# Kernel optimization log

Hardware: AMD Instinct MI355X
Metric: run time of the kernel (lower is better)

Reference implementation:

```python
import jax, jax.numpy as jnp
import numpy as np

E = 8          # num_experts
K = 2          # top_k
R = 16         # lora_r
SCALING = 32.0 / 16.0  # lora_alpha / lora_r

B, S, H, I = 2, 2048, 2048, 8192


def setup_inputs() -> dict:
    key = jax.random.key(0)
    ks = jax.random.split(key, 11)
    inv_h = 1.0 / np.sqrt(H)
    inv_i = 1.0 / np.sqrt(I)
    return {
        "x": jax.random.normal(ks[0], (B, S, H), jnp.float32),
        "gate_W": jax.random.normal(ks[1], (I, H), jnp.float32) * inv_h,
        "up_W": jax.random.normal(ks[2], (I, H), jnp.float32) * inv_h,
        "down_W": jax.random.normal(ks[3], (H, I), jnp.float32) * inv_i,
        "router_W": jax.random.normal(ks[4], (E, H), jnp.float32) * 0.02,
        "gate_A": jax.random.normal(ks[5], (E, R, H), jnp.float32) * inv_h,
        "gate_B": jax.random.normal(ks[6], (E, I, R), jnp.float32) * 0.01,
        "up_A": jax.random.normal(ks[7], (E, R, H), jnp.float32) * inv_h,
        "up_B": jax.random.normal(ks[8], (E, I, R), jnp.float32) * 0.01,
        "down_A": jax.random.normal(ks[9], (E, R, I), jnp.float32) * inv_i,
        "down_B": jax.random.normal(ks[10], (E, H, R), jnp.float32) * 0.01,
    }


def _mixlora_forward(x, gate_W, up_W, down_W, router_W,
                     gate_A, gate_B, up_A, up_B, down_A, down_B):
    b, s, h = x.shape
    T = b * s
    xf = x.reshape(T, h)                                  # [T, H]

    # Shared base FFN projections (computed once for all experts)
    gate_out = xf @ gate_W.T                              # [T, I]
    up_out = xf @ up_W.T                                  # [T, I]

    # Router: softmax in fp32, top-k, renormalize selected weights
    logits = xf @ router_W.T                              # [T, E]
    probs = jax.nn.softmax(logits.astype(jnp.float32), axis=-1)
    w, idx = jax.lax.top_k(probs, K)                      # [T, K]
    w = w / jnp.sum(w, axis=-1, keepdims=True)

    # Dense per-(token, expert) combine weights; 0 for unselected experts
    onehot = jax.nn.one_hot(idx, E, dtype=probs.dtype)    # [T, K, E]
    w_dense = jnp.einsum('tke,tk->te', onehot, w)         # [T, E]

    # Load-balance aux loss: N * sum_i f_i * P_i
    f_i = jnp.sum(onehot, axis=(0, 1)) / T
    p_i = jnp.mean(probs, axis=0)
    aux_loss = E * jnp.dot(f_i, p_i)

    # Scan over experts, accumulating weighted intermediate and down-delta.
    # Since down_proj is linear, sum_k w_k * down(inter_k) = down(sum_k w_k * inter_k).
    def step(carry, p):
        acc_int, acc_dd = carry
        gA, gB, uA, uB, dA, dB, we = p                    # we: [T]
        gd = ((xf @ gA.T) @ gB.T) * SCALING               # [T, I]
        ud = ((xf @ uA.T) @ uB.T) * SCALING               # [T, I]
        inter = jax.nn.silu(gate_out + gd) * (up_out + ud)  # SwiGLU intermediate
        dd = ((inter @ dA.T) @ dB.T) * SCALING            # [T, H]
        we = we.astype(xf.dtype)[:, None]
        return (acc_int + we * inter, acc_dd + we * dd), None

    init = (jnp.zeros((T, gate_W.shape[0]), xf.dtype),
            jnp.zeros((T, h), xf.dtype))
    (acc_int, acc_dd), _ = jax.lax.scan(
        step, init, (gate_A, gate_B, up_A, up_B, down_A, down_B, w_dense.T))

    out = acc_int @ down_W.T + acc_dd                     # [T, H]
    return out.reshape(b, s, h), aux_loss


def reference(x, gate_W, up_W, down_W, router_W,
              gate_A, gate_B, up_A, up_B, down_A, down_B):
    return _mixlora_forward(x, gate_W, up_W, down_W, router_W,
                            gate_A, gate_B, up_A, up_B, down_A, down_B)
```

## Files before the change

### kernel.cpp

```cpp
#include <hip/hip_runtime.h>
#include <stdint.h>
#include <stddef.h>

#define DEVINL __device__ __forceinline__

typedef short sv8 __attribute__((ext_vector_type(8)));
typedef unsigned short usv8 __attribute__((ext_vector_type(8)));
typedef unsigned short usv4 __attribute__((ext_vector_type(4)));
typedef float f32x4 __attribute__((ext_vector_type(4)));

constexpr int T_TOK = 4096;
constexpr int H_DIM = 2048;
constexpr int I_DIM = 8192;
constexpr int E_NUM = 8;
constexpr int R_LORA = 16;
constexpr float SCALING = 2.0f;
constexpr int NQ = 4;
constexpr int TQ = T_TOK / NQ;
constexpr int PQ = TQ * 2;
constexpr int P_TOT = T_TOK * 2;

DEVINL float bf2f(unsigned short u) {
  union { uint32_t i; float f; } v; v.i = ((uint32_t)u) << 16; return v.f;
}
DEVINL unsigned short f2bf(float x) {
  union { float f; uint32_t i; } v; v.f = x;
  uint32_t r = v.i + 0x7FFFu + ((v.i >> 16) & 1u);
  return (unsigned short)(r >> 16);
}
DEVINL float bflo(uint32_t w) {
  union { uint32_t i; float f; } v; v.i = w << 16; return v.f;
}
DEVINL float bfhi(uint32_t w) {
  union { uint32_t i; float f; } v; v.i = w & 0xFFFF0000u; return v.f;
}

DEVINL f32x4 MFMA_BF16(sv8 a, sv8 b, f32x4 c) {
  return __builtin_amdgcn_mfma_f32_16x16x32_bf16(a, b, c, 0, 0, 0);
}

DEVINL void load16_to_lds(const void* g, void* l) {
  __builtin_amdgcn_global_load_lds(
      (const __attribute__((address_space(1))) uint32_t*)g,
      (__attribute__((address_space(3))) uint32_t*)l, 16, 0, 0);
}

#define BARRIER() __builtin_amdgcn_s_barrier()

__global__ void cast_f32_to_bf16(const float4* __restrict__ src, usv4* __restrict__ dst) {
  long i = (long)blockIdx.x * blockDim.x + threadIdx.x;
  float4 v = src[i];
  usv4 o;
  o[0] = f2bf(v.x); o[1] = f2bf(v.y); o[2] = f2bf(v.z); o[3] = f2bf(v.w);
  dst[i] = o;
}

__global__ void cast2_f32_to_bf16(const float4* __restrict__ src0, usv4* __restrict__ dst0,
                                  const float4* __restrict__ src1, usv4* __restrict__ dst1) {
  long i = (long)blockIdx.x * blockDim.x + threadIdx.x;
  const float4* s = blockIdx.y ? src1 : src0;
  usv4* d = blockIdx.y ? dst1 : dst0;
  float4 v = s[i];
  usv4 o;
  o[0] = f2bf(v.x); o[1] = f2bf(v.y); o[2] = f2bf(v.z); o[3] = f2bf(v.w);
  d[i] = o;
}

__global__ void zero_lcnt(int* lcnt) {
  if (threadIdx.x < E_NUM * NQ) lcnt[threadIdx.x] = 0;
}

__global__ void router_kernel(const float* __restrict__ x, const float* __restrict__ rW,
                              float* __restrict__ wbuf, int* __restrict__ idxb,
                              float* __restrict__ probs, int* __restrict__ lcnt,
                              int* __restrict__ lists, unsigned short* __restrict__ xf_bf) {
  const int wave = threadIdx.x >> 6, lane = threadIdx.x & 63;
  const int t = blockIdx.x * 4 + wave;
  const float* xr = x + (long)t * H_DIM;
  unsigned short* xbr = xf_bf + (long)t * H_DIM;
  float acc[E_NUM];
#pragma unroll
  for (int e = 0; e < E_NUM; ++e) acc[e] = 0.f;
  for (int h = lane; h < H_DIM; h += 64) {
    float xv = xr[h];
    xbr[h] = f2bf(xv);
#pragma unroll
    for (int e = 0; e < E_NUM; ++e) acc[e] += xv * rW[e * H_DIM + h];
  }
#pragma unroll
  for (int e = 0; e < E_NUM; ++e) {
#pragma unroll
    for (int off = 32; off; off >>= 1) acc[e] += __shfl_xor(acc[e], off);
  }
  if (lane == 0) {
    float mx = acc[0];
#pragma unroll
    for (int e = 1; e < E_NUM; ++e) mx = fmaxf(mx, acc[e]);
    float p[E_NUM];
    float s = 0.f;
#pragma unroll
    for (int e = 0; e < E_NUM; ++e) { p[e] = expf(acc[e] - mx); s += p[e]; }
    float inv = 1.f / s;
#pragma unroll
    for (int e = 0; e < E_NUM; ++e) p[e] *= inv;
    int e1 = 0;
    for (int e = 1; e < E_NUM; ++e) if (p[e] > p[e1]) e1 = e;
    int e2 = (e1 == 0) ? 1 : 0;
    for (int e = 0; e < E_NUM; ++e) if (e != e1 && p[e] > p[e2]) e2 = e;
    float w1 = p[e1], w2 = p[e2], wsum = w1 + w2;
    wbuf[t * 2 + 0] = w1 / wsum;
    wbuf[t * 2 + 1] = w2 / wsum;
    idxb[t * 2 + 0] = e1;
    idxb[t * 2 + 1] = e2;
#pragma unroll
    for (int e = 0; e < E_NUM; ++e) probs[(long)t * E_NUM + e] = p[e];
    const int q = t / TQ;
    int p1 = atomicAdd(&lcnt[e1 * NQ + q], 1); lists[(e1 * NQ + q) * TQ + p1] = t * 2 + 0;
    int p2 = atomicAdd(&lcnt[e2 * NQ + q], 1); lists[(e2 * NQ + q) * TQ + p2] = t * 2 + 1;
  }
}

__global__ void aux_kernel(const float* __restrict__ probs, const int* __restrict__ lcnt,
                           float* __restrict__ aux_out) {
  const int lane = threadIdx.x;
  float s[E_NUM];
#pragma unroll
  for (int e = 0; e < E_NUM; ++e) s[e] = 0.f;
  for (int t = lane; t < T_TOK; t += 64) {
#pragma unroll
    for (int e = 0; e < E_NUM; ++e) s[e] += probs[(long)t * E_NUM + e];
  }
#pragma unroll
  for (int e = 0; e < E_NUM; ++e) {
#pragma unroll
    for (int off = 32; off; off >>= 1) s[e] += __shfl_xor(s[e], off);
  }
  if (lane == 0) {
    float a = 0.f;
#pragma unroll
    for (int e = 0; e < E_NUM; ++e) {
      int cnt = 0;
#pragma unroll
      for (int q = 0; q < NQ; ++q) cnt += lcnt[e * NQ + q];
      a += ((float)cnt / (float)T_TOK) * (s[e] / (float)T_TOK);
    }
    *aux_out = (float)E_NUM * a;
  }
}

__global__ __launch_bounds__(256)
void lora_a_mfma_kernel(const unsigned short* __restrict__ xf_bf,
                        const unsigned short* __restrict__ gA_bf,
                        const unsigned short* __restrict__ uA_bf,
                        const int* __restrict__ lists, const int* __restrict__ lcnt,
                        float* __restrict__ vg, float* __restrict__ vu) {
  const int q = blockIdx.x / (E_NUM * 16);
  const int rem = blockIdx.x % (E_NUM * 16);
  const int e = rem >> 4;
  const int wave = threadIdx.x >> 6, lane = threadIdx.x & 63;
  const int grp = (rem & 15) * 4 + wave;
  const int npairs = lcnt[e * NQ + q];
  if (grp * 16 >= npairs) return;
  const int* lst = lists + (e * NQ + q) * TQ;
  const int slot = lane & 15;
  int pidx = grp * 16 + slot;
  int pair = lst[(pidx < npairs) ? pidx : grp * 16];
  int t = pair >> 1;
  const long kb = (long)blockIdx.y * 1024 + (lane >> 4) * 8;
  const unsigned short* arow = xf_bf + (long)t * H_DIM + kb;
  const unsigned short* bg = gA_bf + ((long)e * R_LORA + slot) * H_DIM + kb;
  const unsigned short* bu = uA_bf + ((long)e * R_LORA + slot) * H_DIM + kb;
  f32x4 ag = {}, au = {};
#pragma unroll 4
  for (int k = 0; k < 1024; k += 32) {
    sv8 a = *(const sv8*)(arow + k);
    ag = MFMA_BF16(a, *(const sv8*)(bg + k), ag);
    au = MFMA_BF16(a, *(const sv8*)(bu + k), au);
  }
  const int orow = (lane >> 4) * 4;
  const long base = (long)blockIdx.y * P_TOT;
#pragma unroll
  for (int rg = 0; rg < 4; ++rg) {
    int pidx2 = grp * 16 + orow + rg;
    if (pidx2 < npairs) {
      int pr = lst[pidx2];
      vg[(base + pr) * R_LORA + slot] = ag[rg];
      vu[(base + pr) * R_LORA + slot] = au[rg];
    }
  }
}

__global__ void reduce_uguu_kernel(const float* __restrict__ vg, const float* __restrict__ vu,
                                   float* __restrict__ ug, float* __restrict__ uu) {
  long i = (long)blockIdx.x * 256 + threadIdx.x;
  ug[i] = vg[i] + vg[(long)P_TOT * R_LORA + i];
  uu[i] = vu[i] + vu[(long)P_TOT * R_LORA + i];
}

template <bool F32OUT>
__global__ __launch_bounds__(512, 2)
void gemm8p_t(const unsigned short* __restrict__ A,
              const unsigned short* __restrict__ B0,
              const unsigned short* __restrict__ B1,
              unsigned short* __restrict__ Cb0,
              unsigned short* __restrict__ Cb1,
              float* __restrict__ Cf,
              int K, int lda, int ldb, int ldc,
              int az_off, int bz_off, long cz_off) {
  extern __shared__ unsigned short lds[];
  const int z = blockIdx.z;
  const unsigned short* __restrict__ Ap = A + (long)z * az_off;
  const unsigned short* __restrict__ Bp = (z ? B1 : B0) + (long)z * bz_off;
  const int tid = threadIdx.x;
  const int wave = tid >> 6, lane = tid & 63;
  const int wm = wave >> 2, wn = wave & 3;
  const long m0 = (long)blockIdx.y * 256;
  const long n0 = (long)blockIdx.x * 256;
  const int NT = K >> 6;

  const int lr = lane & 15;
  const int lc = (lane >> 4) * 8;
  const int xm = ((lane & 4) << 3) | ((lane & 2) << 3) | ((lane & 1) << 6);
  const int srow = tid >> 3;
  const int scol = (tid & 7) * 8;
  const int gcol = scol ^ (((tid >> 5) & 1) << 4) ^ (((tid >> 4) & 1) << 3)
                        ^ (((tid >> 3) & 1) << 5);

  f32x4 acc[8][4] = {};
  sv8 aF[4][2], bF[4][2];

  auto ldsAt = [&](int buf, int mat) -> unsigned short* {
    return lds + (((buf << 1) + mat) << 14);
  };
  auto stageA = [&](int buf, int R, long k0) {
    load16_to_lds(Ap + (m0 + R + srow) * (long)lda + k0 + gcol,
                  ldsAt(buf, 0) + ((R + srow) << 6) + scol);
  };
  auto stageB = [&](int buf, int R, long k0) {
    load16_to_lds(Bp + (n0 + R + srow) * (long)ldb + k0 + gcol,
                  ldsAt(buf, 1) + ((R + srow) << 6) + scol);
  };
  auto rdA = [&](int buf, int row16, int ks) -> sv8 {
    int bo = ((((row16 + lr) << 7) + ((ks * 32 + lc) << 1))) ^ xm;
    return *(const sv8*)((const char*)ldsAt(buf, 0) + bo);
  };
  auto rdB = [&](int buf, int row16, int ks) -> sv8 {
    int bo = ((((row16 + lr) << 7) + ((ks * 32 + lc) << 1))) ^ xm;
    return *(const sv8*)((const char*)ldsAt(buf, 1) + bo);
  };

  stageA(0, 0, 0); stageA(0, 64, 0); stageA(0, 128, 0); stageA(0, 192, 0);
  stageB(0, 0, 0); stageB(0, 64, 0); stageB(0, 128, 0); stageB(0, 192, 0);
  if (NT > 1) {
    stageA(1, 0, 64); stageA(1, 128, 64);
    asm volatile("s_waitcnt vmcnt(2)" ::: "memory");
  } else {
    asm volatile("s_waitcnt vmcnt(0)" ::: "memory");
  }
  BARRIER();

  for (int t = 0; t < NT; ++t) {
    const int P = t & 1, Q = P ^ 1;
    const long kQ = ((long)t + 1) << 6;
    const long kP2 = ((long)t + 2) << 6;
    const bool hQ = (t + 1) < NT, hP2 = (t + 2) < NT;

#pragma unroll
    for (int mf = 0; mf < 4; ++mf)
#pragma unroll
      for (int ks = 0; ks < 2; ++ks)
        aF[mf][ks] = rdA(P, wm * 128 + mf * 16, ks);
#pragma unroll
    for (int nf = 0; nf < 4; ++nf)
#pragma unroll
      for (int ks = 0; ks < 2; ++ks)
        bF[nf][ks] = rdB(P, wn * 64 + nf * 16, ks);
    if (hQ) { stageA(Q, 64, kQ); stageA(Q, 192, kQ); stageB(Q, 0, kQ); stageB(Q, 64, kQ); }
    __builtin_amdgcn_s_setprio(1);
#pragma unroll
    for (int mf = 0; mf < 4; ++mf)
#pragma unroll
      for (int nf = 0; nf < 4; ++nf)
#pragma unroll
        for (int ks = 0; ks < 2; ++ks)
          acc[mf][nf] = MFMA_BF16(aF[mf][ks], bF[nf][ks], acc[mf][nf]);
    __builtin_amdgcn_s_setprio(0);
    BARRIER();

#pragma unroll
    for (int mf = 0; mf < 4; ++mf)
#pragma unroll
      for (int ks = 0; ks < 2; ++ks)
        aF[mf][ks] = rdA(P, wm * 128 + 64 + mf * 16, ks);
    if (hQ) { stageB(Q, 128, kQ); stageB(Q, 192, kQ); }
    if (hP2) { stageA(P, 0, kP2); stageA(P, 128, kP2); }
    __builtin_amdgcn_s_setprio(1);
#pragma unroll
    for (int mf = 0; mf < 4; ++mf)
#pragma unroll
      for (int nf = 0; nf < 4; ++nf)
#pragma unroll
        for (int ks = 0; ks < 2; ++ks)
          acc[4 + mf][nf] = MFMA_BF16(aF[mf][ks], bF[nf][ks], acc[4 + mf][nf]);
    __builtin_amdgcn_s_setprio(0);
    if (hP2) {
      asm volatile("s_waitcnt vmcnt(2)" ::: "memory");
    } else {
      asm volatile("s_waitcnt vmcnt(0)" ::: "memory");
    }
    BARRIER();
  }

  const int rb = (lane >> 4) * 4, cb = lane & 15;
  if constexpr (F32OUT) {
    float* __restrict__ Cp = Cf + (long)z * cz_off;
#pragma unroll
    for (int mf = 0; mf < 8; ++mf)
#pragma unroll
      for (int nf = 0; nf < 4; ++nf) {
        long col = n0 + wn * 64 + nf * 16 + cb;
#pragma unroll
        for (int r = 0; r < 4; ++r) {
          long row = m0 + wm * 128 + mf * 16 + rb + r;
          Cp[row * ldc + col] = acc[mf][nf][r];
        }
      }
  } else {
    unsigned short* __restrict__ Cp = z ? Cb1 : Cb0;
#pragma unroll
    for (int mf = 0; mf < 8; ++mf)
#pragma unroll
      for (int nf = 0; nf < 4; ++nf) {
        long col = n0 + wn * 64 + nf * 16 + cb;
#pragma unroll
        for (int r = 0; r < 4; ++r) {
          long row = m0 + wm * 128 + mf * 16 + rb + r;
          Cp[row * ldc + col] = f2bf(acc[mf][nf][r]);
        }
      }
  }
}

__global__ __launch_bounds__(256)
void combine2_kernel(const unsigned short* __restrict__ g_bf,
                     const unsigned short* __restrict__ u_bf,
                     const unsigned short* __restrict__ gBp, const unsigned short* __restrict__ uBp,
                     const float* __restrict__ ug, const float* __restrict__ uu,
                     const float* __restrict__ wbuf,
                     const int* __restrict__ lists, const int* __restrict__ lcnt,
                     unsigned short* __restrict__ winter, int q) {
  const int e = blockIdx.y >> 4, chunk = blockIdx.y & 15;
  const int npairs = lcnt[e * NQ + q];
  const int pbase = chunk * 64;
  if (pbase >= npairs) return;
  const int wave = threadIdx.x >> 6, lane = threadIdx.x & 63;
  const long i0 = (long)blockIdx.x * 256 + lane * 4;
  uint32_t gbp[32], ubp[32];
#pragma unroll
  for (int j = 0; j < 4; ++j) {
    const uint4* gp = (const uint4*)(gBp + ((long)e * I_DIM + i0 + j) * R_LORA);
    const uint4* up = (const uint4*)(uBp + ((long)e * I_DIM + i0 + j) * R_LORA);
    uint4 g0 = gp[0], g1 = gp[1], u0 = up[0], u1 = up[1];
    gbp[j * 8 + 0] = g0.x; gbp[j * 8 + 1] = g0.y; gbp[j * 8 + 2] = g0.z; gbp[j * 8 + 3] = g0.w;
    gbp[j * 8 + 4] = g1.x; gbp[j * 8 + 5] = g1.y; gbp[j * 8 + 6] = g1.z; gbp[j * 8 + 7] = g1.w;
    ubp[j * 8 + 0] = u0.x; ubp[j * 8 + 1] = u0.y; ubp[j * 8 + 2] = u0.z; ubp[j * 8 + 3] = u0.w;
    ubp[j * 8 + 4] = u1.x; ubp[j * 8 + 5] = u1.y; ubp[j * 8 + 6] = u1.z; ubp[j * 8 + 7] = u1.w;
  }
  for (int pl = 0; pl < 16; ++pl) {
    int pi = pbase + wave + pl * 4;
    if (pi >= npairs) break;
    int pair = lists[(e * NQ + q) * TQ + pi];
    int t = pair >> 1, plocal = pair - q * PQ;
    float w = wbuf[pair];
    const float2* ug2 = (const float2*)(ug + (long)pair * R_LORA);
    const float2* uu2 = (const float2*)(uu + (long)pair * R_LORA);
    usv4 gv = *(const usv4*)(g_bf + (long)t * I_DIM + i0);
    usv4 uv = *(const usv4*)(u_bf + (long)t * I_DIM + i0);
    float gd[4] = {0.f, 0.f, 0.f, 0.f}, ud[4] = {0.f, 0.f, 0.f, 0.f};
#pragma unroll
    for (int c = 0; c < 8; ++c) {
      float2 a = ug2[c], b = uu2[c];
#pragma unroll
      for (int j = 0; j < 4; ++j) {
        uint32_t gw = gbp[j * 8 + c], uw = ubp[j * 8 + c];
        gd[j] += a.x * bflo(gw) + a.y * bfhi(gw);
        ud[j] += b.x * bflo(uw) + b.y * bfhi(uw);
      }
    }
    usv4 o;
#pragma unroll
    for (int j = 0; j < 4; ++j) {
      float zg = bf2f(gv[j]) + SCALING * gd[j];
      float zu = bf2f(uv[j]) + SCALING * ud[j];
      float sil = zg / (1.f + __expf(-zg));
      o[j] = f2bf(w * sil * zu);
    }
    *(usv4*)(winter + (long)plocal * I_DIM + i0) = o;
  }
}

__global__ void acc_kernel(const unsigned short* __restrict__ winter,
                           unsigned short* __restrict__ acc_bf, int q) {
  long gid = (long)blockIdx.x * 256 + threadIdx.x;
  int tl = (int)(gid >> 10);
  int ig = (int)(gid & 1023);
  int t = q * TQ + tl;
  usv8 a = *(const usv8*)(winter + ((long)(tl * 2 + 0)) * I_DIM + ig * 8);
  usv8 b = *(const usv8*)(winter + ((long)(tl * 2 + 1)) * I_DIM + ig * 8);
  usv8 o;
#pragma unroll
  for (int j = 0; j < 8; ++j) o[j] = f2bf(bf2f(a[j]) + bf2f(b[j]));
  *(usv8*)(acc_bf + (long)t * I_DIM + ig * 8) = o;
}

__global__ __launch_bounds__(256)
void lorav_mfma_kernel(const unsigned short* __restrict__ winter,
                       const unsigned short* __restrict__ dA_bf,
                       const int* __restrict__ lists, const int* __restrict__ lcnt,
                       float* __restrict__ vv, int q) {
  const int e = blockIdx.x >> 4;
  const int wave = threadIdx.x >> 6, lane = threadIdx.x & 63;
  const int grp = (blockIdx.x & 15) * 4 + wave;
  const int npairs = lcnt[e * NQ + q];
  if (grp * 16 >= npairs) return;
  const int* lst = lists + (e * NQ + q) * TQ;
  const int slot = lane & 15;
  int pidx = grp * 16 + slot;
  int pair = lst[(pidx < npairs) ? pidx : grp * 16];
  int plocal = pair - q * PQ;
  const long kb = (long)blockIdx.y * 1024 + (lane >> 4) * 8;
  const unsigned short* arow = winter + (long)plocal * I_DIM + kb;
  const unsigned short* brow = dA_bf + ((long)e * R_LORA + slot) * I_DIM + kb;
  f32x4 acc = {};
#pragma unroll 4
  for (int k = 0; k < 1024; k += 32)
    acc = MFMA_BF16(*(const sv8*)(arow + k), *(const sv8*)(brow + k), acc);
  const int orow = (lane >> 4) * 4;
  const long base = (long)blockIdx.y * P_TOT;
#pragma unroll
  for (int rg = 0; rg < 4; ++rg) {
    int pidx2 = grp * 16 + orow + rg;
    if (pidx2 < npairs) {
      int pr = lst[pidx2];
      vv[(base + pr) * R_LORA + slot] = acc[rg];
    }
  }
}

__global__ void reduce_v_kernel(const float* __restrict__ vv, float* __restrict__ vbuf) {
  long i = (long)blockIdx.x * 256 + threadIdx.x;
  float s = 0.f;
#pragma unroll
  for (int kc = 0; kc < 8; ++kc) s += vv[(long)kc * P_TOT * R_LORA + i];
  vbuf[i] = s;
}

__global__ void ddmerge_kernel(const float* __restrict__ vbuf, const int* __restrict__ idxb,
                               const float* __restrict__ dB,
                               const float* __restrict__ p0, const float* __restrict__ p1,
                               float* __restrict__ out) {
  const int t = blockIdx.y;
  const int h = blockIdx.x * 256 + threadIdx.x;
  const int e0 = idxb[t * 2 + 0], e1 = idxb[t * 2 + 1];
  const float4* v0p = (const float4*)(vbuf + (long)(t * 2 + 0) * R_LORA);
  const float4* v1p = (const float4*)(vbuf + (long)(t * 2 + 1) * R_LORA);
  const float4* b0 = (const float4*)(dB + ((long)e0 * H_DIM + h) * R_LORA);
  const float4* b1 = (const float4*)(dB + ((long)e1 * H_DIM + h) * R_LORA);
  float dd = 0.f;
#pragma unroll
  for (int qq = 0; qq < 4; ++qq) {
    float4 v0 = v0p[qq], x0 = b0[qq];
    float4 v1 = v1p[qq], x1 = b1[qq];
    dd += v0.x * x0.x + v0.y * x0.y + v0.z * x0.z + v0.w * x0.w;
    dd += v1.x * x1.x + v1.y * x1.y + v1.z * x1.z + v1.w * x1.w;
  }
  long i = (long)t * H_DIM + h;
  out[i] = SCALING * dd + p0[i] + p1[i];
}

extern "C" void kernel_launch(void* const* d_in, const int* in_sizes, int n_in,
                              void* d_out, int out_size, void* d_ws, size_t ws_size,
                              hipStream_t stream) {
  (void)in_sizes; (void)n_in; (void)out_size;
  const float* x        = (const float*)d_in[0];
  const float* gate_W   = (const float*)d_in[1];
  const float* up_W     = (const float*)d_in[2];
  const float* down_W   = (const float*)d_in[3];
  const float* router_W = (const float*)d_in[4];
  const float* gate_A   = (const float*)d_in[5];
  const float* gate_B   = (const float*)d_in[6];
  const float* up_A     = (const float*)d_in[7];
  const float* up_B     = (const float*)d_in[8];
  const float* down_A   = (const float*)d_in[9];
  const float* down_B   = (const float*)d_in[10];
  float* out = (float*)d_out;

  char* ws = (char*)d_ws;
  size_t off = 0;
  auto take = [&](size_t bytes) -> char* {
    char* p = ws + off;
    off += (bytes + 255) & ~(size_t)255;
    return p;
  };
  unsigned short* xf_bf  = (unsigned short*)take((size_t)T_TOK * H_DIM * 2);
  unsigned short* gW_bf  = (unsigned short*)take((size_t)I_DIM * H_DIM * 2);
  unsigned short* uW_bf  = (unsigned short*)take((size_t)I_DIM * H_DIM * 2);
  unsigned short* dA_bf  = (unsigned short*)take((size_t)E_NUM * R_LORA * I_DIM * 2);
  unsigned short* g_bf   = (unsigned short*)take((size_t)T_TOK * I_DIM * 2);
  unsigned short* u_bf   = (unsigned short*)take((size_t)T_TOK * I_DIM * 2);
  unsigned short* winterQ= (unsigned short*)take((size_t)PQ * I_DIM * 2);
  float* wbuf  = (float*)take((size_t)P_TOT * 4);
  int*   idxb  = (int*)take((size_t)P_TOT * 4);
  float* ug    = (float*)take((size_t)P_TOT * R_LORA * 4);
  float* uu    = (float*)take((size_t)P_TOT * R_LORA * 4);
  float* vbuf  = (float*)take((size_t)P_TOT * R_LORA * 4);
  float* probs = (float*)take((size_t)T_TOK * E_NUM * 4);
  int*   lcnt  = (int*)take((size_t)E_NUM * NQ * 4);
  int*   lists = (int*)take((size_t)E_NUM * NQ * TQ * 4);

  unsigned short* dW_bf  = gW_bf;
  unsigned short* acc_bf = g_bf;
  float* vg = (float*)winterQ;
  float* vu = (float*)(winterQ + (size_t)1 * 1024 * 1024 / 2);
  unsigned short* gA_bf = winterQ + (size_t)2 * 1024 * 1024 / 2;
  unsigned short* uA_bf = winterQ + (size_t)5 * 512 * 1024 / 2;
  float* vv = (float*)xf_bf;
  unsigned short* gB_bf = (unsigned short*)((char*)xf_bf + ((size_t)4 << 20));
  unsigned short* uB_bf = (unsigned short*)((char*)xf_bf + ((size_t)8 << 20));
  float* pbuf = (float*)u_bf;

  if (ws_size < off) return;

  zero_lcnt<<<1, 64, 0, stream>>>(lcnt);
  router_kernel<<<T_TOK / 4, 256, 0, stream>>>(x, router_W, wbuf, idxb, probs, lcnt, lists, xf_bf);
  aux_kernel<<<1, 64, 0, stream>>>(probs, lcnt, out + (size_t)T_TOK * H_DIM);

  cast2_f32_to_bf16<<<dim3((E_NUM * R_LORA * H_DIM / 4) / 256, 2), 256, 0, stream>>>(
      (const float4*)gate_A, (usv4*)gA_bf, (const float4*)up_A, (usv4*)uA_bf);
  lora_a_mfma_kernel<<<dim3(NQ * E_NUM * 16, 2), 256, 0, stream>>>(xf_bf, gA_bf, uA_bf, lists, lcnt, vg, vu);
  reduce_uguu_kernel<<<(P_TOT * R_LORA) / 256, 256, 0, stream>>>(vg, vu, ug, uu);

  cast2_f32_to_bf16<<<dim3((I_DIM * H_DIM / 4) / 256, 2), 256, 0, stream>>>(
      (const float4*)gate_W, (usv4*)gW_bf, (const float4*)up_W, (usv4*)uW_bf);
  cast_f32_to_bf16<<<(E_NUM * R_LORA * I_DIM / 4) / 256, 256, 0, stream>>>((const float4*)down_A, (usv4*)dA_bf);

  hipFuncSetAttribute(reinterpret_cast<const void*>(&gemm8p_t<false>),
                      hipFuncAttributeMaxDynamicSharedMemorySize, 131072);
  hipFuncSetAttribute(reinterpret_cast<const void*>(&gemm8p_t<true>),
                      hipFuncAttributeMaxDynamicSharedMemorySize, 131072);
  gemm8p_t<false><<<dim3(I_DIM / 256, T_TOK / 256, 2), 512, 131072, stream>>>(
      xf_bf, gW_bf, uW_bf, g_bf, u_bf, nullptr,
      H_DIM, H_DIM, H_DIM, I_DIM, 0, 0, 0);

  cast_f32_to_bf16<<<(H_DIM * I_DIM / 4) / 256, 256, 0, stream>>>((const float4*)down_W, (usv4*)dW_bf);
  cast2_f32_to_bf16<<<dim3((E_NUM * I_DIM * R_LORA / 4) / 256, 2), 256, 0, stream>>>(
      (const float4*)gate_B, (usv4*)gB_bf, (const float4*)up_B, (usv4*)uB_bf);

  for (int q = 0; q < NQ; ++q) {
    combine2_kernel<<<dim3(I_DIM / 256, E_NUM * 16), 256, 0, stream>>>(
        g_bf, u_bf, gB_bf, uB_bf, ug, uu, wbuf, lists, lcnt, winterQ, q);
    acc_kernel<<<(TQ * (I_DIM / 8)) / 256, 256, 0, stream>>>(winterQ, acc_bf, q);
    lorav_mfma_kernel<<<dim3(E_NUM * 16, 8), 256, 0, stream>>>(winterQ, dA_bf, lists, lcnt, vv, q);
  }
  reduce_v_kernel<<<(P_TOT * R_LORA) / 256, 256, 0, stream>>>(vv, vbuf);

  gemm8p_t<true><<<dim3(H_DIM / 256, T_TOK / 256, 2), 512, 131072, stream>>>(
      acc_bf, dW_bf, dW_bf, nullptr, nullptr, pbuf,
      I_DIM / 2, I_DIM, I_DIM, H_DIM, I_DIM / 2, I_DIM / 2, (long)T_TOK * H_DIM);

  ddmerge_kernel<<<dim3(H_DIM / 256, T_TOK), 256, 0, stream>>>(
      vbuf, idxb, down_B, (const float*)pbuf,
      (const float*)(pbuf + (size_t)T_TOK * H_DIM), out);
}
```

Before: 1.043 ms.

## Batch token quarters into single launches and issue all B-tile loads earlier

When the workspace is large enough, the combine, accumulate and LoRA-down kernels now process all four token quarters in one launch each, using blockIdx.z and a winter buffer that is four times larger. This replaces twelve small launches with three larger ones. It cuts launch overhead and the idle gaps between kernels, and it gives each launch more parallel work. The GEMM mainloop also issues all four B-tile stage loads in the first half of each iteration instead of splitting them across the two halves, which changes how prefetch overlaps with the MFMA work.

Measured after the change: 1.039 ms. Within noise of the previous version (-0.3%).

```diff
diff --git a/kernel.cpp b/kernel.cpp
--- a/kernel.cpp
+++ b/kernel.cpp
@@ -275,7 +275,10 @@
 #pragma unroll
       for (int ks = 0; ks < 2; ++ks)
         bF[nf][ks] = rdB(P, wn * 64 + nf * 16, ks);
-    if (hQ) { stageA(Q, 64, kQ); stageA(Q, 192, kQ); stageB(Q, 0, kQ); stageB(Q, 64, kQ); }
+    if (hQ) {
+      stageA(Q, 64, kQ); stageA(Q, 192, kQ);
+      stageB(Q, 0, kQ); stageB(Q, 64, kQ); stageB(Q, 128, kQ); stageB(Q, 192, kQ);
+    }
     __builtin_amdgcn_s_setprio(1);
 #pragma unroll
     for (int mf = 0; mf < 4; ++mf)
@@ -292,7 +295,6 @@
 #pragma unroll
       for (int ks = 0; ks < 2; ++ks)
         aF[mf][ks] = rdA(P, wm * 128 + 64 + mf * 16, ks);
-    if (hQ) { stageB(Q, 128, kQ); stageB(Q, 192, kQ); }
     if (hP2) { stageA(P, 0, kP2); stageA(P, 128, kP2); }
     __builtin_amdgcn_s_setprio(1);
 #pragma unroll
@@ -348,7 +350,10 @@
                      const float* __restrict__ ug, const float* __restrict__ uu,
                      const float* __restrict__ wbuf,
                      const int* __restrict__ lists, const int* __restrict__ lcnt,
-                     unsigned short* __restrict__ winter, int q) {
+                     unsigned short* __restrict__ winter, int q0) {
+  const int zq = blockIdx.z;
+  const int q = q0 + zq;
+  unsigned short* __restrict__ wint = winter + (size_t)zq * PQ * I_DIM;
   const int e = blockIdx.y >> 4, chunk = blockIdx.y & 15;
   const int npairs = lcnt[e * NQ + q];
   const int pbase = chunk * 64;
@@ -395,18 +400,20 @@
       float sil = zg / (1.f + __expf(-zg));
       o[j] = f2bf(w * sil * zu);
     }
-    *(usv4*)(winter + (long)plocal * I_DIM + i0) = o;
+    *(usv4*)(wint + (long)plocal * I_DIM + i0) = o;
   }
 }
 
 __global__ void acc_kernel(const unsigned short* __restrict__ winter,
-                           unsigned short* __restrict__ acc_bf, int q) {
+                           unsigned short* __restrict__ acc_bf, int q0) {
+  const int zq = blockIdx.z;
+  const unsigned short* __restrict__ wint = winter + (size_t)zq * PQ * I_DIM;
   long gid = (long)blockIdx.x * 256 + threadIdx.x;
   int tl = (int)(gid >> 10);
   int ig = (int)(gid & 1023);
-  int t = q * TQ + tl;
-  usv8 a = *(const usv8*)(winter + ((long)(tl * 2 + 0)) * I_DIM + ig * 8);
-  usv8 b = *(const usv8*)(winter + ((long)(tl * 2 + 1)) * I_DIM + ig * 8);
+  int t = (q0 + zq) * TQ + tl;
+  usv8 a = *(const usv8*)(wint + ((long)(tl * 2 + 0)) * I_DIM + ig * 8);
+  usv8 b = *(const usv8*)(wint + ((long)(tl * 2 + 1)) * I_DIM + ig * 8);
   usv8 o;
 #pragma unroll
   for (int j = 0; j < 8; ++j) o[j] = f2bf(bf2f(a[j]) + bf2f(b[j]));
@@ -417,7 +424,10 @@
 void lorav_mfma_kernel(const unsigned short* __restrict__ winter,
                        const unsigned short* __restrict__ dA_bf,
                        const int* __restrict__ lists, const int* __restrict__ lcnt,
-                       float* __restrict__ vv, int q) {
+                       float* __restrict__ vv, int q0) {
+  const int zq = blockIdx.z;
+  const int q = q0 + zq;
+  const unsigned short* __restrict__ wint = winter + (size_t)zq * PQ * I_DIM;
   const int e = blockIdx.x >> 4;
   const int wave = threadIdx.x >> 6, lane = threadIdx.x & 63;
   const int grp = (blockIdx.x & 15) * 4 + wave;
@@ -429,7 +439,7 @@
   int pair = lst[(pidx < npairs) ? pidx : grp * 16];
   int plocal = pair - q * PQ;
   const long kb = (long)blockIdx.y * 1024 + (lane >> 4) * 8;
-  const unsigned short* arow = winter + (long)plocal * I_DIM + kb;
+  const unsigned short* arow = wint + (long)plocal * I_DIM + kb;
   const unsigned short* brow = dA_bf + ((long)e * R_LORA + slot) * I_DIM + kb;
   f32x4 acc = {};
 #pragma unroll 4
@@ -508,7 +518,6 @@
   unsigned short* dA_bf  = (unsigned short*)take((size_t)E_NUM * R_LORA * I_DIM * 2);
   unsigned short* g_bf   = (unsigned short*)take((size_t)T_TOK * I_DIM * 2);
   unsigned short* u_bf   = (unsigned short*)take((size_t)T_TOK * I_DIM * 2);
-  unsigned short* winterQ= (unsigned short*)take((size_t)PQ * I_DIM * 2);
   float* wbuf  = (float*)take((size_t)P_TOT * 4);
   int*   idxb  = (int*)take((size_t)P_TOT * 4);
   float* ug    = (float*)take((size_t)P_TOT * R_LORA * 4);
@@ -517,6 +526,10 @@
   float* probs = (float*)take((size_t)T_TOK * E_NUM * 4);
   int*   lcnt  = (int*)take((size_t)E_NUM * NQ * 4);
   int*   lists = (int*)take((size_t)E_NUM * NQ * TQ * 4);
+  const size_t qwin = (size_t)PQ * I_DIM * 2;
+  size_t fixed = off;
+  int QB = (ws_size >= fixed + 4 * qwin) ? 4 : 1;
+  unsigned short* winterQ = (unsigned short*)take(qwin * QB);
 
   unsigned short* dW_bf  = gW_bf;
   unsigned short* acc_bf = g_bf;
@@ -556,11 +569,11 @@
   cast2_f32_to_bf16<<<dim3((E_NUM * I_DIM * R_LORA / 4) / 256, 2), 256, 0, stream>>>(
       (const float4*)gate_B, (usv4*)gB_bf, (const float4*)up_B, (usv4*)uB_bf);
 
-  for (int q = 0; q < NQ; ++q) {
-    combine2_kernel<<<dim3(I_DIM / 256, E_NUM * 16), 256, 0, stream>>>(
-        g_bf, u_bf, gB_bf, uB_bf, ug, uu, wbuf, lists, lcnt, winterQ, q);
-    acc_kernel<<<(TQ * (I_DIM / 8)) / 256, 256, 0, stream>>>(winterQ, acc_bf, q);
-    lorav_mfma_kernel<<<dim3(E_NUM * 16, 8), 256, 0, stream>>>(winterQ, dA_bf, lists, lcnt, vv, q);
+  for (int q0 = 0; q0 < NQ; q0 += QB) {
+    combine2_kernel<<<dim3(I_DIM / 256, E_NUM * 16, QB), 256, 0, stream>>>(
+        g_bf, u_bf, gB_bf, uB_bf, ug, uu, wbuf, lists, lcnt, winterQ, q0);
+    acc_kernel<<<dim3((TQ * (I_DIM / 8)) / 256, 1, QB), 256, 0, stream>>>(winterQ, acc_bf, q0);
+    lorav_mfma_kernel<<<dim3(E_NUM * 16, 8, QB), 256, 0, stream>>>(winterQ, dA_bf, lists, lcnt, vv, q0);
   }
   reduce_v_kernel<<<(P_TOT * R_LORA) / 256, 256, 0, stream>>>(vv, vbuf);
 
```
